# Performance work log

Measured on AMD Instinct MI355X. Metric: run time of the kernel, lower is better.

Reference implementation:

```python
import jax, jax.numpy as jnp
import numpy as np

NUM_EXPERTS = 8
D_MODEL = 768
D_FF = 4 * D_MODEL


def setup_inputs() -> dict:
    key = jax.random.key(0)
    ks = jax.random.split(key, 7)
    s = 0.02
    x = jax.random.normal(ks[0], (2, 1024, D_MODEL), dtype=jnp.float32)
    router_w = jax.random.normal(ks[1], (D_MODEL, NUM_EXPERTS), dtype=jnp.float32) * s
    router_b = jnp.zeros((NUM_EXPERTS,), dtype=jnp.float32)
    w1 = jax.random.normal(ks[2], (NUM_EXPERTS, D_MODEL, D_FF), dtype=jnp.float32) * s
    b1 = jnp.zeros((NUM_EXPERTS, D_FF), dtype=jnp.float32)
    w2 = jax.random.normal(ks[3], (NUM_EXPERTS, D_FF, D_MODEL), dtype=jnp.float32) * s
    b2 = jnp.zeros((NUM_EXPERTS, D_MODEL), dtype=jnp.float32)
    return {"x": x, "router_w": router_w, "router_b": router_b,
            "w1": w1, "b1": b1, "w2": w2, "b2": b2}


def reference(x, router_w, router_b, w1, b1, w2, b2):
    B, S, D = x.shape
    x_flat = x.reshape(-1, D)                      # [T, D]
    logits = x_flat @ router_w + router_b          # [T, E]
    probs = jax.nn.softmax(logits, axis=-1)
    expert_idx = jnp.argmax(probs, axis=-1)        # [T] int, top-1 routing
    onehot = jax.nn.one_hot(expert_idx, NUM_EXPERTS, dtype=x.dtype)  # [T, E]

    # Per-expert FFN; combine via top-1 one-hot (output is NOT scaled by prob,
    # matching the original). Dropout is eval-mode identity.
    out = jnp.zeros_like(x_flat)
    for e in range(NUM_EXPERTS):
        h = jax.nn.relu(x_flat @ w1[e] + b1[e])    # [T, D_FF]
        y = h @ w2[e] + b2[e]                      # [T, D]
        out = out + onehot[:, e:e + 1] * y
    outputs = out.reshape(B, S, D)

    # Load-balance loss: MSE between empirical expert usage and uniform.
    usage = jnp.bincount(expert_idx, length=NUM_EXPERTS).astype(jnp.float32)
    usage = usage / usage.sum()
    uniform = jnp.full((NUM_EXPERTS,), 1.0 / NUM_EXPERTS, dtype=jnp.float32)
    load_balance_loss = jnp.mean((usage - uniform) ** 2)
    return outputs, load_balance_loss
```

## Files before the change

kernel.cpp:

```cpp
#include <hip/hip_runtime.h>
#include <hip/hip_bf16.h>

#define NTOK 2048
#define DMODEL 768
#define DFF 3072
#define NEXP 8
#define MAXT 40

typedef short bf16x8 __attribute__((ext_vector_type(8)));
typedef float f32x4 __attribute__((ext_vector_type(4)));

typedef __attribute__((address_space(1))) const char GCHAR;
typedef __attribute__((address_space(3))) char LCHAR;
#define GL16(g, l) __builtin_amdgcn_global_load_lds((GCHAR*)(g), (LCHAR*)(l), 16, 0, 0)

template <int K, int N>
__device__ void transpose32(const float* __restrict__ W, __hip_bfloat16* __restrict__ WT,
                            int e, int k0, int n0, float* T) {
  const int t = threadIdx.x;
#pragma unroll
  for (int i = 0; i < 2; i++) {
    const int idx = t + i * 256;
    const int kr = idx >> 4;
    const int c4 = (idx & 15) * 4;
    float4 v = *(const float4*)(W + ((size_t)e * K + k0 + kr) * N + n0 + c4);
    T[kr * 65 + c4 + 0] = v.x;
    T[kr * 65 + c4 + 1] = v.y;
    T[kr * 65 + c4 + 2] = v.z;
    T[kr * 65 + c4 + 3] = v.w;
  }
  __syncthreads();
  const int n = t >> 2;
  const int kc = (t & 3) * 8;
  __align__(16) __hip_bfloat16 u[8];
#pragma unroll
  for (int j = 0; j < 8; j++) u[j] = __float2bfloat16(T[(kc + j) * 65 + n]);
  *(int4*)(WT + ((size_t)e * N + n0 + n) * K + k0 + kc) = *(const int4*)u;
}

__global__ __launch_bounds__(256, 4) void k_router_t1(
    const float* __restrict__ x, const float* __restrict__ rw,
    const float* __restrict__ rb, __hip_bfloat16* __restrict__ xbf,
    int* __restrict__ eidx, int* __restrict__ cnt,
    const float* __restrict__ w1, __hip_bfloat16* __restrict__ wT1) {
  __shared__ float T[32 * 65];
  if (blockIdx.x >= 512) {
    int tb = blockIdx.x - 512;
    int n_i = tb % (DFF / 64);
    int k_i = (tb / (DFF / 64)) % (DMODEL / 32);
    int e = tb / ((DFF / 64) * (DMODEL / 32));
    transpose32<DMODEL, DFF>(w1, wT1, e, k_i * 32, n_i * 64, T);
    return;
  }
  int tok = (blockIdx.x * blockDim.x + threadIdx.x) >> 6;
  int lane = threadIdx.x & 63;
  if (tok >= NTOK) return;
  const float* xr = x + (size_t)tok * DMODEL;
  double acc[NEXP];
#pragma unroll
  for (int e = 0; e < NEXP; e++) acc[e] = 0.0;
  for (int d0 = 0; d0 < DMODEL; d0 += 64) {
    float v = xr[d0 + lane];
    xbf[(size_t)tok * DMODEL + d0 + lane] = __float2bfloat16(v);
    const float* wrow = rw + (size_t)(d0 + lane) * NEXP;
#pragma unroll
    for (int e = 0; e < NEXP; e++) acc[e] += (double)v * (double)wrow[e];
  }
#pragma unroll
  for (int e = 0; e < NEXP; e++) {
    double a = acc[e];
#pragma unroll
    for (int s = 32; s > 0; s >>= 1) a += __shfl_xor(a, s);
    acc[e] = a;
  }
  if (lane == 0) {
    int best = 0;
    double bv = acc[0] + (double)rb[0];
#pragma unroll
    for (int e = 1; e < NEXP; e++) {
      double v = acc[e] + (double)rb[e];
      if (v > bv) { bv = v; best = e; }
    }
    eidx[tok] = best;
    atomicAdd(&cnt[best], 1);
  }
}

__global__ void k_scan(const int* __restrict__ cnt, int* __restrict__ off,
                       int* __restrict__ cur, float* __restrict__ loss,
                       int* __restrict__ tiles, int* __restrict__ ntile) {
  if (threadIdx.x == 0) {
    int s = 0;
    float l = 0.f;
    int nt = 0;
    for (int e = 0; e < NEXP; e++) {
      off[e] = s;
      cur[e] = s;
      for (int m = 0; m < cnt[e]; m += 64) tiles[nt++] = (e << 20) | m;
      s += cnt[e];
      float u = (float)cnt[e] / (float)NTOK - 1.0f / (float)NEXP;
      l += u * u;
    }
    *ntile = nt;
    *loss = l / (float)NEXP;
  }
}

__global__ __launch_bounds__(256) void k_build(const int* __restrict__ eidx,
                                               int* __restrict__ cur,
                                               int* __restrict__ list) {
  int t = blockIdx.x * blockDim.x + threadIdx.x;
  if (t < NTOK) {
    int e = eidx[t];
    int p = atomicAdd(&cur[e], 1);
    list[p] = t;
  }
}

template <int K_TOT, int KCHUNK, int N, int NSPLIT, bool RELU_BF16, bool GATHER_A,
          int TK, int TN>
__global__ __launch_bounds__(256, 6) void k_gemm9(
    const __hip_bfloat16* __restrict__ A, const __hip_bfloat16* __restrict__ BT,
    const float* __restrict__ bias, void* __restrict__ Cout,
    const int* __restrict__ cnt, const int* __restrict__ off,
    const int* __restrict__ list, const int* __restrict__ tiles,
    const int* __restrict__ ntile, const float* __restrict__ Tsrc,
    __hip_bfloat16* __restrict__ Tdst) {
  constexpr int NX = N / 128;
  constexpr int W = NX * MAXT * NSPLIT;
  constexpr int NT = KCHUNK / 32;
  __shared__ __align__(16) char smem[24576];

  if constexpr (TK > 0) {
    if (blockIdx.x >= W) {
      int tb = blockIdx.x - W;
      int n_i = tb % (TN / 64);
      int k_i = (tb / (TN / 64)) % (TK / 32);
      int e = tb / ((TN / 64) * (TK / 32));
      transpose32<TK, TN>(Tsrc, Tdst, e, k_i * 32, n_i * 64, (float*)smem);
      return;
    }
  }

  int b = blockIdx.x;
  constexpr int q = W / 8, r = W % 8;
  const int xcd = b & 7, ii = b >> 3;
  const int widx = (xcd < r ? xcd * (q + 1) : r * (q + 1) + (xcd - r) * q) + ii;
  const int split = widx % NSPLIT;
  const int rest = widx / NSPLIT;
  const int ti = rest % MAXT;
  const int nx = rest / MAXT;
  if (ti >= *ntile) return;
  const int tv = tiles[ti];
  const int e = tv >> 20;
  const int m0 = tv & 0xFFFFF;
  const int ce = cnt[e];
  const int oe = off[e];
  const int n0 = nx * 128;
  const int kbase = split * KCHUNK;

  const int tid = threadIdx.x;
  const int lane = tid & 63;
  const int w = tid >> 6;
  const int wr = (w >> 1) * 32;
  const int wc = (w & 1) * 64;
  const int fr = lane & 15;
  const int hi = lane >> 4;
  const int xr = (fr >> 1) & 3;

  const int srow = tid >> 2;
  const int cch = (tid & 3) ^ ((tid >> 3) & 3);

  const __hip_bfloat16* ga;
  {
    int mr = m0 + srow;
    int src;
    if (GATHER_A) {
      src = list[oe + (mr < ce ? mr : 0)];
    } else {
      int p2 = oe + mr;
      src = p2 < NTOK ? p2 : NTOK - 1;
    }
    ga = A + (size_t)src * K_TOT + kbase + cch * 8;
  }
  const __hip_bfloat16* gb[2];
#pragma unroll
  for (int j = 0; j < 2; j++) {
    int nr = n0 + j * 64 + srow;
    gb[j] = BT + ((size_t)e * N + nr) * K_TOT + kbase + cch * 8;
  }

  f32x4 acc[2][4] = {};

#define STAGE(buf, kc)                                              \
  do {                                                              \
    GL16(ga + (kc), smem + (buf)*4096 + tid * 16);                  \
    GL16(gb[0] + (kc), smem + 8192 + (buf)*8192 + tid * 16);        \
    GL16(gb[1] + (kc), smem + 8192 + (buf)*8192 + 4096 + tid * 16); \
  } while (0)

  STAGE(0, 0);
#pragma unroll 1
  for (int t = 0; t < NT; ++t) {
    if (t + 1 < NT) {
      STAGE((t + 1) & 1, (t + 1) * 32);
      asm volatile("s_waitcnt vmcnt(3)" ::: "memory");
    } else {
      asm volatile("s_waitcnt vmcnt(0)" ::: "memory");
    }
    __builtin_amdgcn_s_barrier();
    {
      const char* bA = smem + (t & 1) * 4096;
      const char* bB = smem + 8192 + (t & 1) * 8192;
      bf16x8 fa[2], fb[4];
#pragma unroll
      for (int mf = 0; mf < 2; mf++) {
        const int row = wr + mf * 16 + fr;
        fa[mf] = *(const bf16x8*)(bA + row * 64 + ((hi ^ xr) * 16));
      }
#pragma unroll
      for (int nf = 0; nf < 4; nf++) {
        const int row = wc + nf * 16 + fr;
        fb[nf] = *(const bf16x8*)(bB + row * 64 + ((hi ^ xr) * 16));
      }
#pragma unroll
      for (int mf = 0; mf < 2; mf++)
#pragma unroll
        for (int nf = 0; nf < 4; nf++)
          acc[mf][nf] = __builtin_amdgcn_mfma_f32_16x16x32_bf16(fa[mf], fb[nf],
                                                                acc[mf][nf], 0, 0, 0);
    }
    __builtin_amdgcn_s_barrier();
  }
#undef STAGE

#pragma unroll
  for (int mf = 0; mf < 2; mf++) {
#pragma unroll
    for (int jj = 0; jj < 4; jj++) {
      const int mloc = m0 + wr + mf * 16 + hi * 4 + jj;
      if (mloc >= ce) continue;
      if (RELU_BF16) {
        __hip_bfloat16* C = (__hip_bfloat16*)Cout;
        size_t row = (size_t)(oe + mloc) * N;
        const float* bi = bias + (size_t)e * N;
#pragma unroll
        for (int nf = 0; nf < 4; nf++) {
          int nn = n0 + wc + nf * 16 + fr;
          float v = acc[mf][nf][jj] + bi[nn];
          C[row + nn] = __float2bfloat16(v > 0.f ? v : 0.f);
        }
      } else {
        float* C = (float*)Cout;
        int tok = list[oe + mloc];
        size_t row = ((size_t)split * NTOK + tok) * N;
#pragma unroll
        for (int nf = 0; nf < 4; nf++) {
          int nn = n0 + wc + nf * 16 + fr;
          C[row + nn] = acc[mf][nf][jj];
        }
      }
    }
  }
}

__global__ __launch_bounds__(256) void k_reduce(const float* __restrict__ p,
                                                const float* __restrict__ b2,
                                                const int* __restrict__ eidx,
                                                float* __restrict__ out) {
  const int idx = blockIdx.x * 256 + threadIdx.x;
  const int base = idx * 4;
  const int tok = base / DMODEL;
  const int n = base - tok * DMODEL;
  const int e = eidx[tok];
  float4 a = *(const float4*)(p + (size_t)0 * NTOK * DMODEL + base);
  float4 c = *(const float4*)(p + (size_t)1 * NTOK * DMODEL + base);
  float4 d = *(const float4*)(p + (size_t)2 * NTOK * DMODEL + base);
  float4 g = *(const float4*)(p + (size_t)3 * NTOK * DMODEL + base);
  float4 bb = *(const float4*)(b2 + (size_t)e * DMODEL + n);
  float4 o;
  o.x = a.x + c.x + d.x + g.x + bb.x;
  o.y = a.y + c.y + d.y + g.y + bb.y;
  o.z = a.z + c.z + d.z + g.z + bb.z;
  o.w = a.w + c.w + d.w + g.w + bb.w;
  *(float4*)(out + base) = o;
}

template <int K, int N, bool RELU_BF16, bool GATHER_A, bool SCATTER_C>
__global__ __launch_bounds__(256) void k_gemm(
    const __hip_bfloat16* __restrict__ A, const float* __restrict__ Bw,
    const float* __restrict__ bias, void* __restrict__ Cout,
    const int* __restrict__ cnt, const int* __restrict__ off,
    const int* __restrict__ list) {
  const int e = blockIdx.z;
  const int ce = cnt[e];
  const int m0 = blockIdx.y * 128;
  if (m0 >= ce) return;
  const int oe = off[e];
  const int n0 = blockIdx.x * 128;

  __shared__ __hip_bfloat16 Asm[128][32];
  __shared__ __hip_bfloat16 Bsm[128][32];

  const int tid = threadIdx.x;
  const int ra = tid >> 1;
  const int ha = (tid & 1) * 16;
  size_t arow;
  {
    int mr = m0 + ra;
    int src;
    if (GATHER_A) {
      src = (mr < ce) ? list[oe + mr] : list[oe];
    } else {
      int p = oe + mr;
      src = (p < NTOK) ? p : (NTOK - 1);
    }
    arow = (size_t)src * K;
  }
  const int rbk = tid >> 3;
  const int nb = (tid & 7) * 16;
  const float* bsrc0 = Bw + ((size_t)e * K + rbk) * N + n0 + nb;

  const int w = tid >> 6;
  const int lane = tid & 63;
  const int wr = (w >> 1) * 64;
  const int wc = (w & 1) * 64;
  const int fr = lane & 15;
  const int fk = (lane >> 4) * 8;

  f32x4 acc[4][4] = {};

  for (int k0 = 0; k0 < K; k0 += 32) {
    __syncthreads();
    {
      const __hip_bfloat16* s = A + arow + k0 + ha;
      int4 v0 = *(const int4*)(s);
      int4 v1 = *(const int4*)(s + 8);
      *(int4*)(&Asm[ra][ha]) = v0;
      *(int4*)(&Asm[ra][ha + 8]) = v1;
    }
    {
      const float* s = bsrc0 + (size_t)k0 * N;
      float4 q0 = *(const float4*)(s);
      float4 q1 = *(const float4*)(s + 4);
      float4 q2 = *(const float4*)(s + 8);
      float4 q3 = *(const float4*)(s + 12);
      __hip_bfloat16* dst = &Bsm[nb][0] + rbk;
      dst[0 * 32] = __float2bfloat16(q0.x);
      dst[1 * 32] = __float2bfloat16(q0.y);
      dst[2 * 32] = __float2bfloat16(q0.z);
      dst[3 * 32] = __float2bfloat16(q0.w);
      dst[4 * 32] = __float2bfloat16(q1.x);
      dst[5 * 32] = __float2bfloat16(q1.y);
      dst[6 * 32] = __float2bfloat16(q1.z);
      dst[7 * 32] = __float2bfloat16(q1.w);
      dst[8 * 32] = __float2bfloat16(q2.x);
      dst[9 * 32] = __float2bfloat16(q2.y);
      dst[10 * 32] = __float2bfloat16(q2.z);
      dst[11 * 32] = __float2bfloat16(q2.w);
      dst[12 * 32] = __float2bfloat16(q3.x);
      dst[13 * 32] = __float2bfloat16(q3.y);
      dst[14 * 32] = __float2bfloat16(q3.z);
      dst[15 * 32] = __float2bfloat16(q3.w);
    }
    __syncthreads();

    bf16x8 fa[4], fb[4];
#pragma unroll
    for (int mf = 0; mf < 4; mf++) fa[mf] = *(const bf16x8*)(&Asm[wr + mf * 16 + fr][fk]);
#pragma unroll
    for (int nf = 0; nf < 4; nf++) fb[nf] = *(const bf16x8*)(&Bsm[wc + nf * 16 + fr][fk]);
#pragma unroll
    for (int mf = 0; mf < 4; mf++)
#pragma unroll
      for (int nf = 0; nf < 4; nf++)
        acc[mf][nf] = __builtin_amdgcn_mfma_f32_16x16x32_bf16(fa[mf], fb[nf], acc[mf][nf], 0, 0, 0);
  }

#pragma unroll
  for (int mf = 0; mf < 4; mf++) {
#pragma unroll
    for (int j = 0; j < 4; j++) {
      const int mloc = m0 + wr + mf * 16 + (lane >> 4) * 4 + j;
      if (mloc >= ce) continue;
      if (RELU_BF16) {
        __hip_bfloat16* C = (__hip_bfloat16*)Cout;
        size_t row = (size_t)(oe + mloc) * N;
        const float* bi = bias + (size_t)e * N;
#pragma unroll
        for (int nf = 0; nf < 4; nf++) {
          int nn = n0 + wc + nf * 16 + fr;
          float v = acc[mf][nf][j] + bi[nn];
          C[row + nn] = __float2bfloat16(v > 0.f ? v : 0.f);
        }
      } else {
        float* C = (float*)Cout;
        int tok = SCATTER_C ? list[oe + mloc] : (oe + mloc);
        size_t row = (size_t)tok * N;
        const float* bi = bias + (size_t)e * N;
#pragma unroll
        for (int nf = 0; nf < 4; nf++) {
          int nn = n0 + wc + nf * 16 + fr;
          C[row + nn] = acc[mf][nf][j] + bi[nn];
        }
      }
    }
  }
}

extern "C" void kernel_launch(void* const* d_in, const int* in_sizes, int n_in,
                              void* d_out, int out_size, void* d_ws, size_t ws_size,
                              hipStream_t stream) {
  const float* x = (const float*)d_in[0];
  const float* rw = (const float*)d_in[1];
  const float* rb = (const float*)d_in[2];
  const float* w1 = (const float*)d_in[3];
  const float* b1 = (const float*)d_in[4];
  const float* w2 = (const float*)d_in[5];
  const float* b2 = (const float*)d_in[6];
  float* out = (float*)d_out;

  char* ws = (char*)d_ws;
  int* cnt = (int*)(ws + 0);
  int* off = (int*)(ws + 32);
  int* cur = (int*)(ws + 64);
  int* ntile = (int*)(ws + 96);
  int* tiles = (int*)(ws + 128);
  int* eidx = (int*)(ws + 512);
  int* list = (int*)(ws + 8704);
  __hip_bfloat16* xbf = (__hip_bfloat16*)(ws + 65536);
  __hip_bfloat16* h = (__hip_bfloat16*)(ws + 4194304);
  __hip_bfloat16* wT1 = (__hip_bfloat16*)(ws + 20971520);
  float* part = (float*)(ws + 20971520);
  __hip_bfloat16* wT2 = (__hip_bfloat16*)(ws + 58720256);

  float* loss = out + (size_t)2 * 1024 * 768;
  const size_t REQ = 58720256ull + 37748736ull;

  (void)hipMemsetAsync(cnt, 0, 96, stream);
  if (ws_size < REQ)
    (void)hipMemsetAsync(d_out, 0, (size_t)out_size * sizeof(float), stream);

  if (ws_size >= REQ) {
    const int T1BLK = (DMODEL / 32) * (DFF / 64) * NEXP;
    const int T2BLK = (DFF / 32) * (DMODEL / 64) * NEXP;
    k_router_t1<<<512 + T1BLK, 256, 0, stream>>>(x, rw, rb, xbf, eidx, cnt, w1, wT1);
    k_scan<<<1, 64, 0, stream>>>(cnt, off, cur, loss, tiles, ntile);
    k_build<<<8, 256, 0, stream>>>(eidx, cur, list);
    k_gemm9<DMODEL, DMODEL, DFF, 1, true, true, DFF, DMODEL>
        <<<(DFF / 128) * MAXT + T2BLK, 256, 0, stream>>>(
            xbf, wT1, b1, h, cnt, off, list, tiles, ntile, w2, wT2);
    k_gemm9<DFF, DFF / 4, DMODEL, 4, false, false, 0, 64>
        <<<(DMODEL / 128) * MAXT * 4, 256, 0, stream>>>(
            h, wT2, nullptr, part, cnt, off, list, tiles, ntile, nullptr, nullptr);
    k_reduce<<<(NTOK * DMODEL) / 1024, 256, 0, stream>>>(part, b2, eidx, out);
  } else {
    k_router_t1<<<512, 256, 0, stream>>>(x, rw, rb, xbf, eidx, cnt, w1, nullptr);
    k_scan<<<1, 64, 0, stream>>>(cnt, off, cur, loss, tiles, ntile);
    k_build<<<8, 256, 0, stream>>>(eidx, cur, list);
    k_gemm<DMODEL, DFF, true, true, false>
        <<<dim3(DFF / 128, 16, NEXP), 256, 0, stream>>>(xbf, w1, b1, h, cnt, off, list);
    k_gemm<DFF, DMODEL, false, false, true>
        <<<dim3(DMODEL / 128, 16, NEXP), 256, 0, stream>>>(h, w2, b2, out, cnt, off, list);
  }
}
```

Before: 140.8 us.

## Fuse split-K reduction into GEMM via atomics and enlarge weight transpose tiles

The second expert GEMM now accumulates its four split-K partials straight into the zeroed output with float atomicAdd, adding bias only in split 0. This removes the partial-sum buffer and the separate reduce kernel. The weight transpose-to-bf16 helper now handles 64x64 tiles instead of 32x64, halving the number of transpose blocks while giving each thread more work. In exchange the whole output is memset every call, atomic contention is added, and the summation order becomes nondeterministic.

```diff
diff --git a/kernel.cpp b/kernel.cpp
--- a/kernel.cpp
+++ b/kernel.cpp
@@ -15,41 +15,47 @@
 #define GL16(g, l) __builtin_amdgcn_global_load_lds((GCHAR*)(g), (LCHAR*)(l), 16, 0, 0)
 
 template <int K, int N>
-__device__ void transpose32(const float* __restrict__ W, __hip_bfloat16* __restrict__ WT,
-                            int e, int k0, int n0, float* T) {
+__device__ void transpose_tile(const float* __restrict__ W, __hip_bfloat16* __restrict__ WT,
+                               int e, int k0, int n0, float* T) {
   const int t = threadIdx.x;
-#pragma unroll
-  for (int i = 0; i < 2; i++) {
-    const int idx = t + i * 256;
-    const int kr = idx >> 4;
-    const int c4 = (idx & 15) * 4;
-    float4 v = *(const float4*)(W + ((size_t)e * K + k0 + kr) * N + n0 + c4);
-    T[kr * 65 + c4 + 0] = v.x;
-    T[kr * 65 + c4 + 1] = v.y;
-    T[kr * 65 + c4 + 2] = v.z;
-    T[kr * 65 + c4 + 3] = v.w;
+  {
+    const int kr = t >> 4;
+    const int nc = (t & 15) * 4;
+    const float* src = W + ((size_t)e * K + k0) * N + n0;
+#pragma unroll
+    for (int i = 0; i < 4; i++) {
+      float4 v = *(const float4*)(src + (size_t)(kr + i * 16) * N + nc);
+      T[(kr + i * 16) * 65 + nc + 0] = v.x;
+      T[(kr + i * 16) * 65 + nc + 1] = v.y;
+      T[(kr + i * 16) * 65 + nc + 2] = v.z;
+      T[(kr + i * 16) * 65 + nc + 3] = v.w;
+    }
   }
   __syncthreads();
-  const int n = t >> 2;
-  const int kc = (t & 3) * 8;
-  __align__(16) __hip_bfloat16 u[8];
-#pragma unroll
-  for (int j = 0; j < 8; j++) u[j] = __float2bfloat16(T[(kc + j) * 65 + n]);
-  *(int4*)(WT + ((size_t)e * N + n0 + n) * K + k0 + kc) = *(const int4*)u;
-}
-
-__global__ __launch_bounds__(256, 4) void k_router_t1(
+  {
+    const int n = t >> 2;
+    const int kq = (t & 3) * 16;
+    __align__(16) __hip_bfloat16 u[16];
+#pragma unroll
+    for (int j = 0; j < 16; j++) u[j] = __float2bfloat16(T[(kq + j) * 65 + n]);
+    __hip_bfloat16* dst = WT + ((size_t)e * N + n0 + n) * K + k0 + kq;
+    *(int4*)dst = *(const int4*)&u[0];
+    *(int4*)(dst + 8) = *(const int4*)&u[8];
+  }
+}
+
+__global__ __launch_bounds__(256) void k_router_t1(
     const float* __restrict__ x, const float* __restrict__ rw,
     const float* __restrict__ rb, __hip_bfloat16* __restrict__ xbf,
     int* __restrict__ eidx, int* __restrict__ cnt,
     const float* __restrict__ w1, __hip_bfloat16* __restrict__ wT1) {
-  __shared__ float T[32 * 65];
+  __shared__ float T[64 * 65];
   if (blockIdx.x >= 512) {
     int tb = blockIdx.x - 512;
     int n_i = tb % (DFF / 64);
-    int k_i = (tb / (DFF / 64)) % (DMODEL / 32);
-    int e = tb / ((DFF / 64) * (DMODEL / 32));
-    transpose32<DMODEL, DFF>(w1, wT1, e, k_i * 32, n_i * 64, T);
+    int k_i = (tb / (DFF / 64)) % (DMODEL / 64);
+    int e = tb / ((DFF / 64) * (DMODEL / 64));
+    transpose_tile<DMODEL, DFF>(w1, wT1, e, k_i * 64, n_i * 64, T);
     return;
   }
   int tok = (blockIdx.x * blockDim.x + threadIdx.x) >> 6;
@@ -118,8 +124,8 @@
 }
 
 template <int K_TOT, int KCHUNK, int N, int NSPLIT, bool RELU_BF16, bool GATHER_A,
-          int TK, int TN>
-__global__ __launch_bounds__(256, 6) void k_gemm9(
+          bool ATOMIC_C, int TK, int TN>
+__global__ __launch_bounds__(256, 6) void k_gemm10(
     const __hip_bfloat16* __restrict__ A, const __hip_bfloat16* __restrict__ BT,
     const float* __restrict__ bias, void* __restrict__ Cout,
     const int* __restrict__ cnt, const int* __restrict__ off,
@@ -135,9 +141,9 @@
     if (blockIdx.x >= W) {
       int tb = blockIdx.x - W;
       int n_i = tb % (TN / 64);
-      int k_i = (tb / (TN / 64)) % (TK / 32);
-      int e = tb / ((TN / 64) * (TK / 32));
-      transpose32<TK, TN>(Tsrc, Tdst, e, k_i * 32, n_i * 64, (float*)smem);
+      int k_i = (tb / (TN / 64)) % (TK / 64);
+      int e = tb / ((TN / 64) * (TK / 64));
+      transpose_tile<TK, TN>(Tsrc, Tdst, e, k_i * 64, n_i * 64, (float*)smem);
       return;
     }
   }
@@ -253,37 +259,20 @@
       } else {
         float* C = (float*)Cout;
         int tok = list[oe + mloc];
-        size_t row = ((size_t)split * NTOK + tok) * N;
+        size_t row = (size_t)tok * N;
+        const float* bi = bias + (size_t)e * N;
 #pragma unroll
         for (int nf = 0; nf < 4; nf++) {
           int nn = n0 + wc + nf * 16 + fr;
-          C[row + nn] = acc[mf][nf][jj];
+          float v = acc[mf][nf][jj] + (split == 0 ? bi[nn] : 0.f);
+          if (ATOMIC_C)
+            atomicAdd(&C[row + nn], v);
+          else
+            C[row + nn] = v;
         }
       }
     }
   }
-}
-
-__global__ __launch_bounds__(256) void k_reduce(const float* __restrict__ p,
-                                                const float* __restrict__ b2,
-                                                const int* __restrict__ eidx,
-                                                float* __restrict__ out) {
-  const int idx = blockIdx.x * 256 + threadIdx.x;
-  const int base = idx * 4;
-  const int tok = base / DMODEL;
-  const int n = base - tok * DMODEL;
-  const int e = eidx[tok];
-  float4 a = *(const float4*)(p + (size_t)0 * NTOK * DMODEL + base);
-  float4 c = *(const float4*)(p + (size_t)1 * NTOK * DMODEL + base);
-  float4 d = *(const float4*)(p + (size_t)2 * NTOK * DMODEL + base);
-  float4 g = *(const float4*)(p + (size_t)3 * NTOK * DMODEL + base);
-  float4 bb = *(const float4*)(b2 + (size_t)e * DMODEL + n);
-  float4 o;
-  o.x = a.x + c.x + d.x + g.x + bb.x;
-  o.y = a.y + c.y + d.y + g.y + bb.y;
-  o.z = a.z + c.z + d.z + g.z + bb.z;
-  o.w = a.w + c.w + d.w + g.w + bb.w;
-  *(float4*)(out + base) = o;
 }
 
 template <int K, int N, bool RELU_BF16, bool GATHER_A, bool SCATTER_C>
@@ -431,29 +420,25 @@
   __hip_bfloat16* xbf = (__hip_bfloat16*)(ws + 65536);
   __hip_bfloat16* h = (__hip_bfloat16*)(ws + 4194304);
   __hip_bfloat16* wT1 = (__hip_bfloat16*)(ws + 20971520);
-  float* part = (float*)(ws + 20971520);
   __hip_bfloat16* wT2 = (__hip_bfloat16*)(ws + 58720256);
 
   float* loss = out + (size_t)2 * 1024 * 768;
   const size_t REQ = 58720256ull + 37748736ull;
 
   (void)hipMemsetAsync(cnt, 0, 96, stream);
-  if (ws_size < REQ)
-    (void)hipMemsetAsync(d_out, 0, (size_t)out_size * sizeof(float), stream);
+  (void)hipMemsetAsync(d_out, 0, (size_t)out_size * sizeof(float), stream);
 
   if (ws_size >= REQ) {
-    const int T1BLK = (DMODEL / 32) * (DFF / 64) * NEXP;
-    const int T2BLK = (DFF / 32) * (DMODEL / 64) * NEXP;
-    k_router_t1<<<512 + T1BLK, 256, 0, stream>>>(x, rw, rb, xbf, eidx, cnt, w1, wT1);
+    const int TBLK = (DMODEL / 64) * (DFF / 64) * NEXP;
+    k_router_t1<<<512 + TBLK, 256, 0, stream>>>(x, rw, rb, xbf, eidx, cnt, w1, wT1);
     k_scan<<<1, 64, 0, stream>>>(cnt, off, cur, loss, tiles, ntile);
     k_build<<<8, 256, 0, stream>>>(eidx, cur, list);
-    k_gemm9<DMODEL, DMODEL, DFF, 1, true, true, DFF, DMODEL>
-        <<<(DFF / 128) * MAXT + T2BLK, 256, 0, stream>>>(
+    k_gemm10<DMODEL, DMODEL, DFF, 1, true, true, false, DFF, DMODEL>
+        <<<(DFF / 128) * MAXT + TBLK, 256, 0, stream>>>(
             xbf, wT1, b1, h, cnt, off, list, tiles, ntile, w2, wT2);
-    k_gemm9<DFF, DFF / 4, DMODEL, 4, false, false, 0, 64>
+    k_gemm10<DFF, DFF / 4, DMODEL, 4, false, false, true, 0, 64>
         <<<(DMODEL / 128) * MAXT * 4, 256, 0, stream>>>(
-            h, wT2, nullptr, part, cnt, off, list, tiles, ntile, nullptr, nullptr);
-    k_reduce<<<(NTOK * DMODEL) / 1024, 256, 0, stream>>>(part, b2, eidx, out);
+            h, wT2, b2, out, cnt, off, list, tiles, ntile, nullptr, nullptr);
   } else {
     k_router_t1<<<512, 256, 0, stream>>>(x, rw, rb, xbf, eidx, cnt, w1, nullptr);
     k_scan<<<1, 64, 0, stream>>>(cnt, off, cur, loss, tiles, ntile);
```

Measured after the change: 148.8 us. 5.7% more time.
